# Optimization experiments

Hardware: AMD Instinct MI355X
Metric: run time of the kernel (lower is better)

Reference implementation:

```python
import jax, jax.numpy as jnp
import numpy as np

N, E, G, H, IN = 200000, 400000, 64, 128, 5
LN_EPS = 1e-5


def setup_inputs() -> dict:
    key = jax.random.key(0)
    ks = jax.random.split(key, 32)
    d = {}
    d["x"] = jax.random.normal(ks[0], (N, IN), jnp.float32)
    d["edge_index"] = jax.random.randint(ks[1], (2, E), 0, N, dtype=jnp.int32)
    d["edge_attr"] = jax.random.normal(ks[2], (E, 1), jnp.float32)
    d["batch"] = jnp.sort(jax.random.randint(ks[3], (N,), 0, G, dtype=jnp.int32))
    dims = [IN, H, H]
    i = 4
    names = [("ew", "eb", "w1_", "b1_", "w2_", "b2_", "g", "bt")]
    for l, din in enumerate(dims):
        d[f"ew{l}"] = jax.random.normal(ks[i], (1, din), jnp.float32); i += 1
        d[f"eb{l}"] = jnp.zeros((din,), jnp.float32)
        d[f"w1_{l}"] = jax.random.normal(ks[i], (din, H), jnp.float32) / np.sqrt(din); i += 1
        d[f"b1_{l}"] = jnp.zeros((H,), jnp.float32)
        d[f"w2_{l}"] = jax.random.normal(ks[i], (H, H), jnp.float32) / np.sqrt(H); i += 1
        d[f"b2_{l}"] = jnp.zeros((H,), jnp.float32)
        d[f"g{l}"] = jnp.ones((H,), jnp.float32)
        d[f"bt{l}"] = jnp.zeros((H,), jnp.float32)
    return d


def _gine_layer(x, src, dst, edge_attr, ew, eb, w1, b1, w2, b2, g, bt):
    # edge encoder: Linear(1, din)
    e = edge_attr @ ew + eb                       # [E, din]
    # GINEConv message: ReLU(x_j + e), aggregated (sum) at destination
    m = jax.nn.relu(x[src] + e)                   # [E, din]
    aggr = jax.ops.segment_sum(m, dst, num_segments=N)  # [N, din]
    h = x + aggr                                  # (1 + eps)*x with eps=0
    # GIN MLP: Linear -> ReLU -> Linear
    h = jax.nn.relu(h @ w1 + b1) @ w2 + b2        # [N, H]
    # LayerNorm
    mu = jnp.mean(h, axis=-1, keepdims=True)
    var = jnp.mean((h - mu) ** 2, axis=-1, keepdims=True)
    h = (h - mu) * jax.lax.rsqrt(var + LN_EPS) * g + bt
    return jax.nn.relu(h)


def reference(x, edge_index, edge_attr, batch,
              ew0, eb0, w1_0, b1_0, w2_0, b2_0, g0, bt0,
              ew1, eb1, w1_1, b1_1, w2_1, b2_1, g1, bt1,
              ew2, eb2, w1_2, b1_2, w2_2, b2_2, g2, bt2):
    src, dst = edge_index[0], edge_index[1]
    x = _gine_layer(x, src, dst, edge_attr, ew0, eb0, w1_0, b1_0, w2_0, b2_0, g0, bt0)
    x = _gine_layer(x, src, dst, edge_attr, ew1, eb1, w1_1, b1_1, w2_1, b2_1, g1, bt1)
    x = _gine_layer(x, src, dst, edge_attr, ew2, eb2, w1_2, b1_2, w2_2, b2_2, g2, bt2)
    # global pooling per graph
    add_pool = jax.ops.segment_sum(x, batch, num_segments=G)           # [G, H]
    counts = jax.ops.segment_sum(jnp.ones((N,), x.dtype), batch, num_segments=G)
    mean_pool = add_pool / jnp.maximum(counts, 1.0)[:, None]           # [G, H]
    return jnp.concatenate([mean_pool, add_pool], axis=1)              # [G, 2H]
```

## Files before the change

### kernel.cpp

```cpp
#include <hip/hip_runtime.h>

#define N_NODES 200000
#define N_EDGES 400000
#define N_GRAPHS 64
#define HDIM 128
#define INDIM 5
#define LN_EPS 1e-5f
#define LDA 138
#define NPBLK 64

typedef __attribute__((ext_vector_type(8))) short short8;
typedef __attribute__((ext_vector_type(4))) float f32x4;

__device__ __forceinline__ unsigned short to_bf(float v) {
    unsigned u = __builtin_bit_cast(unsigned, v);
    return (unsigned short)((u + 0x7FFFu + ((u >> 16) & 1u)) >> 16);
}
__device__ __forceinline__ float bf_lo(unsigned w) { return __builtin_bit_cast(float, w << 16); }
__device__ __forceinline__ float bf_hi(unsigned w) { return __builtin_bit_cast(float, w & 0xFFFF0000u); }
__device__ __forceinline__ float bf2f(unsigned short h) { return __builtin_bit_cast(float, (unsigned)h << 16); }


__global__ void hist_kernel(const int* __restrict__ ei, int* __restrict__ deg) {
    int e = blockIdx.x * blockDim.x + threadIdx.x;
    if (e < N_EDGES) atomicAdd(&deg[ei[N_EDGES + e]], 1);
}

#define SCAN_CHUNK 1024
#define SCAN_BLOCKS ((N_NODES + SCAN_CHUNK - 1) / SCAN_CHUNK)

__global__ __launch_bounds__(256) void scan_phaseA(const int* __restrict__ deg, int* __restrict__ bsums,
                                                   int* __restrict__ poolz) {
    if (blockIdx.x == 0) {
        for (int i = threadIdx.x; i < N_GRAPHS * HDIM + N_GRAPHS; i += 256) poolz[i] = 0;
    }
    __shared__ int red[256];
    int t = threadIdx.x;
    int base = blockIdx.x * SCAN_CHUNK + t * 4;
    int s = 0;
#pragma unroll
    for (int k = 0; k < 4; ++k) {
        int i = base + k;
        s += (i < N_NODES) ? deg[i] : 0;
    }
    red[t] = s;
    __syncthreads();
    for (int off = 128; off; off >>= 1) {
        if (t < off) red[t] += red[t + off];
        __syncthreads();
    }
    if (t == 0) bsums[blockIdx.x] = red[0];
}

__global__ __launch_bounds__(256) void scan_phaseB(int* __restrict__ bsums, int* __restrict__ row_ptr) {
    __shared__ int s[256];
    int t = threadIdx.x;
    int v = (t < SCAN_BLOCKS) ? bsums[t] : 0;
    s[t] = v;
    __syncthreads();
    for (int off = 1; off < 256; off <<= 1) {
        int add = (t >= off) ? s[t - off] : 0;
        __syncthreads();
        s[t] += add;
        __syncthreads();
    }
    if (t < SCAN_BLOCKS) bsums[t] = s[t] - v;
    if (t == SCAN_BLOCKS - 1) row_ptr[N_NODES] = s[t];
}

__global__ __launch_bounds__(256) void scan_phaseC(const int* __restrict__ deg,
                                                   const int* __restrict__ bsums,
                                                   int* __restrict__ row_ptr,
                                                   int* __restrict__ cursor) {
    __shared__ int ts[256];
    int t = threadIdx.x;
    int base = blockIdx.x * SCAN_CHUNK + t * 4;
    int v[4];
    int s = 0;
#pragma unroll
    for (int k = 0; k < 4; ++k) {
        int i = base + k;
        v[k] = (i < N_NODES) ? deg[i] : 0;
        s += v[k];
    }
    ts[t] = s;
    __syncthreads();
    for (int off = 1; off < 256; off <<= 1) {
        int add = (t >= off) ? ts[t - off] : 0;
        __syncthreads();
        ts[t] += add;
        __syncthreads();
    }
    int run = bsums[blockIdx.x] + ts[t] - s;
#pragma unroll
    for (int k = 0; k < 4; ++k) {
        int i = base + k;
        if (i < N_NODES) { row_ptr[i] = run; cursor[i] = 0; }
        run += v[k];
    }
}

#define SCATTER_BLOCKS ((N_EDGES + 255) / 256)

__global__ void scatter_pack(const int* __restrict__ ei, const float* __restrict__ ea,
                             const int* __restrict__ row_ptr, int* __restrict__ cursor,
                             int2* __restrict__ csr,
                             const float* __restrict__ s0, short* __restrict__ d0,
                             const float* __restrict__ s1, short* __restrict__ d1,
                             const float* __restrict__ s2, short* __restrict__ d2,
                             const float* __restrict__ s3, short* __restrict__ d3,
                             const float* __restrict__ s4, short* __restrict__ d4,
                             const float* __restrict__ s5, short* __restrict__ d5) {
    int b = blockIdx.x;
    if (b < SCATTER_BLOCKS) {
        int e = b * 256 + threadIdx.x;
        if (e >= N_EDGES) return;
        int d = ei[N_EDGES + e];
        int pos = atomicAdd(&cursor[d], 1);
        csr[row_ptr[d] + pos] = make_int2(ei[e], __float_as_int(ea[e]));
        return;
    }
    b -= SCATTER_BLOCKS;
    const float* W;
    short* D;
    int din, KP, b0;
    if (b < 16)       { W = s0; D = d0; din = 5;   KP = 32;  b0 = 0; }
    else if (b < 80)  { W = s1; D = d1; din = 128; KP = 128; b0 = 16; }
    else if (b < 144) { W = s2; D = d2; din = 128; KP = 128; b0 = 80; }
    else if (b < 208) { W = s3; D = d3; din = 128; KP = 128; b0 = 144; }
    else if (b < 272) { W = s4; D = d4; din = 128; KP = 128; b0 = 208; }
    else              { W = s5; D = d5; din = 128; KP = 128; b0 = 272; }
    int idx = (b - b0) * 256 + threadIdx.x;
    if (idx >= KP * 128) return;
    int j = idx & 7;
    int lane = (idx >> 3) & 63;
    int rest = idx >> 9;
    int KS = KP >> 5;
    int kstep = rest % KS;
    int tile = rest / KS;
    int k = kstep * 32 + ((lane >> 4) * 8) + j;
    int n = tile * 16 + (lane & 15);
    float v = (k < din) ? W[k * 128 + n] : 0.f;
    D[idx] = (short)to_bf(v);
}

template <int KP1, bool POOL>
__global__ __launch_bounds__(256, 4) void layer_fused(
    const void* __restrict__ xin_v, const int* __restrict__ row_ptr,
    const int2* __restrict__ csr,
    const float* __restrict__ ew, const float* __restrict__ eb,
    const short* __restrict__ w1h, const float* __restrict__ b1,
    const short* __restrict__ w2h, const float* __restrict__ b2,
    const float* __restrict__ g, const float* __restrict__ bt,
    unsigned short* __restrict__ xout,
    const int* __restrict__ batch, float* __restrict__ pool, int* __restrict__ cnt) {
    __shared__ __align__(16) unsigned short A16[NPBLK * LDA];
    __shared__ int bidx[NPBLK];
    union Scratch {
        float eweb[256];
        float part[NPBLK][4][INDIM];
    };
    __shared__ Scratch u;

    int tid = threadIdx.x;
    int node0 = blockIdx.x * NPBLK;

    if (KP1 == 128) {
        const unsigned short* xin = (const unsigned short*)xin_v;
        if (tid < 32) ((float4*)u.eweb)[tid] = ((const float4*)ew)[tid];
        else if (tid < 64) ((float4*)u.eweb)[tid] = ((const float4*)eb)[tid - 32];
        if (POOL && tid >= 64 && tid < 128) bidx[tid - 64] = batch[node0 + tid - 64];

        int row = tid >> 2, qt = tid & 3, c0 = qt * 32;
        int node = node0 + row;
        float acc[32];
        {
            const uint4* xn = (const uint4*)(xin + (size_t)node * 128 + c0);
            uint4 uv[4];
#pragma unroll
            for (int j = 0; j < 4; ++j) uv[j] = xn[j];
            unsigned wds[16] = {uv[0].x, uv[0].y, uv[0].z, uv[0].w,
                                uv[1].x, uv[1].y, uv[1].z, uv[1].w,
                                uv[2].x, uv[2].y, uv[2].z, uv[2].w,
                                uv[3].x, uv[3].y, uv[3].z, uv[3].w};
#pragma unroll
            for (int i = 0; i < 16; ++i) {
                acc[2 * i] = bf_lo(wds[i]);
                acc[2 * i + 1] = bf_hi(wds[i]);
            }
        }
        int beg = row_ptr[node], end = row_ptr[node + 1];
        __syncthreads();

        int2 r;
        if (beg < end) r = csr[beg];
        for (int e = beg; e < end; ++e) {
            int2 rn = (e + 1 < end) ? csr[e + 1] : r;
            float a = __int_as_float(r.y);
            const uint4* xs = (const uint4*)(xin + (size_t)r.x * 128 + c0);
            uint4 uv[4];
#pragma unroll
            for (int j = 0; j < 4; ++j) uv[j] = xs[j];
            unsigned wds[16] = {uv[0].x, uv[0].y, uv[0].z, uv[0].w,
                                uv[1].x, uv[1].y, uv[1].z, uv[1].w,
                                uv[2].x, uv[2].y, uv[2].z, uv[2].w,
                                uv[3].x, uv[3].y, uv[3].z, uv[3].w};
#pragma unroll
            for (int i = 0; i < 16; ++i) {
                int cA = c0 + 2 * i, cB = cA + 1;
                acc[2 * i] += fmaxf(fmaf(a, u.eweb[cA], bf_lo(wds[i]) + u.eweb[128 + cA]), 0.f);
                acc[2 * i + 1] += fmaxf(fmaf(a, u.eweb[cB], bf_hi(wds[i]) + u.eweb[128 + cB]), 0.f);
            }
            r = rn;
        }
        unsigned* Ar = (unsigned*)&A16[row * LDA + c0];
#pragma unroll
        for (int i = 0; i < 16; ++i)
            Ar[i] = (unsigned)to_bf(acc[2 * i]) | ((unsigned)to_bf(acc[2 * i + 1]) << 16);
    } else {
        const float* xinf = (const float*)xin_v;
        int row = tid >> 2, qt = tid & 3;
        int node = node0 + row;
        {
            float w[INDIM], b[INDIM], acc[INDIM];
#pragma unroll
            for (int j = 0; j < INDIM; ++j) {
                w[j] = ew[j];
                b[j] = eb[j];
                acc[j] = 0.f;
            }
            int beg = row_ptr[node], end = row_ptr[node + 1];
            int2 r;
            if (beg + qt < end) r = csr[beg + qt];
            for (int e = beg + qt; e < end; e += 4) {
                int2 rn = (e + 4 < end) ? csr[e + 4] : r;
                float a = __int_as_float(r.y);
#pragma unroll
                for (int j = 0; j < INDIM; ++j)
                    acc[j] += fmaxf(fmaf(a, w[j], xinf[r.x * INDIM + j] + b[j]), 0.f);
                r = rn;
            }
#pragma unroll
            for (int j = 0; j < INDIM; ++j) u.part[row][qt][j] = acc[j];
        }
        __syncthreads();
        if (tid < NPBLK) {
#pragma unroll
            for (int j = 0; j < INDIM; ++j) {
                float v = xinf[(node0 + tid) * INDIM + j] + u.part[tid][0][j] + u.part[tid][1][j] +
                          u.part[tid][2][j] + u.part[tid][3][j];
                A16[tid * LDA + j] = to_bf(v);
            }
#pragma unroll
            for (int j = INDIM; j < 32; ++j) A16[tid * LDA + j] = 0;
        }
        __syncthreads();
    }

    int wv = tid >> 6, lane = tid & 63;
    int mrow = lane & 15, q = lane >> 4;
    int arow = wv * 16 + mrow;

    const short8* w1p = (const short8*)w1h;
    const short8* w2p = (const short8*)w2h;

    f32x4 acc2[8];
#pragma unroll
    for (int t = 0; t < 8; ++t) acc2[t] = (f32x4){0.f, 0.f, 0.f, 0.f};
    constexpr int KS1 = KP1 / 32;
#pragma unroll
    for (int ks = 0; ks < KS1; ++ks) {
        short8 bh[8];
#pragma unroll
        for (int t = 0; t < 8; ++t) bh[t] = w1p[((size_t)t * KS1 + ks) * 64 + lane];
        short8 ah = *(const short8*)&A16[arow * LDA + ks * 32 + q * 8];
#pragma unroll
        for (int t = 0; t < 8; ++t)
            acc2[t] = __builtin_amdgcn_mfma_f32_16x16x32_bf16(ah, bh[t], acc2[t], 0, 0, 0);
    }
    {
        float b1v[8];
#pragma unroll
        for (int t = 0; t < 8; ++t) b1v[t] = b1[t * 16 + mrow];
#pragma unroll
        for (int t = 0; t < 8; ++t)
#pragma unroll
            for (int r = 0; r < 4; ++r) {
                int rrow = wv * 16 + q * 4 + r;
                int col = t * 16 + mrow;
                A16[rrow * LDA + col] = to_bf(fmaxf(acc2[t][r] + b1v[t], 0.f));
            }
    }

#pragma unroll
    for (int t = 0; t < 8; ++t) acc2[t] = (f32x4){0.f, 0.f, 0.f, 0.f};
#pragma unroll
    for (int ks = 0; ks < 4; ++ks) {
        short8 bh[8];
#pragma unroll
        for (int t = 0; t < 8; ++t) bh[t] = w2p[((size_t)t * 4 + ks) * 64 + lane];
        short8 ah = *(const short8*)&A16[arow * LDA + ks * 32 + q * 8];
#pragma unroll
        for (int t = 0; t < 8; ++t)
            acc2[t] = __builtin_amdgcn_mfma_f32_16x16x32_bf16(ah, bh[t], acc2[t], 0, 0, 0);
    }

    float s4[4] = {0.f, 0.f, 0.f, 0.f}, q4[4] = {0.f, 0.f, 0.f, 0.f};
    {
        float b2v[8];
#pragma unroll
        for (int t = 0; t < 8; ++t) b2v[t] = b2[t * 16 + mrow];
#pragma unroll
        for (int t = 0; t < 8; ++t)
#pragma unroll
            for (int r = 0; r < 4; ++r) {
                float v = acc2[t][r] + b2v[t];
                acc2[t][r] = v;
                s4[r] += v;
                q4[r] += v * v;
            }
    }
#pragma unroll
    for (int m = 1; m <= 8; m <<= 1) {
#pragma unroll
        for (int r = 0; r < 4; ++r) {
            s4[r] += __shfl_xor(s4[r], m, 64);
            q4[r] += __shfl_xor(q4[r], m, 64);
        }
    }
    float mu[4], inv[4];
#pragma unroll
    for (int r = 0; r < 4; ++r) {
        mu[r] = s4[r] * (1.f / HDIM);
        float var = q4[r] * (1.f / HDIM) - mu[r] * mu[r];
        inv[r] = rsqrtf(var + LN_EPS);
    }
    float gv[8], btv[8];
#pragma unroll
    for (int t = 0; t < 8; ++t) {
        gv[t] = g[t * 16 + mrow];
        btv[t] = bt[t * 16 + mrow];
    }

#pragma unroll
    for (int t = 0; t < 8; ++t)
#pragma unroll
        for (int r = 0; r < 4; ++r) {
            int rrow = wv * 16 + q * 4 + r;
            int col = t * 16 + mrow;
            float o = fmaxf((acc2[t][r] - mu[r]) * inv[r] * gv[t] + btv[t], 0.f);
            A16[rrow * LDA + col] = to_bf(o);
        }
    __syncthreads();

    if (!POOL) {
        unsigned* xo = (unsigned*)xout;
#pragma unroll
        for (int i = 0; i < 16; ++i) {
            int idx = tid + 256 * i;
            int row = idx >> 6, w = idx & 63;
            xo[(size_t)(node0 + row) * 64 + w] = ((const unsigned*)&A16[row * LDA])[w];
        }
    } else {
        if (tid < 128) {
            int col = tid;
            float accp = 0.f;
            int cur = bidx[0];
            for (int r = 0; r < NPBLK; ++r) {
                int gi = bidx[r];
                if (gi != cur) {
                    unsafeAtomicAdd(&pool[cur * HDIM + col], accp);
                    accp = 0.f;
                    cur = gi;
                }
                accp += bf2f(A16[r * LDA + col]);
            }
            unsafeAtomicAdd(&pool[cur * HDIM + col], accp);
        } else if (tid == 255) {
            int cur = bidx[0], c = 0;
            for (int r = 0; r < NPBLK; ++r) {
                if (bidx[r] != cur) {
                    atomicAdd(&cnt[cur], c);
                    c = 0;
                    cur = bidx[r];
                }
                ++c;
            }
            atomicAdd(&cnt[cur], c);
        }
    }
}

__global__ void pool_final(const float* __restrict__ pool, const int* __restrict__ cnt,
                           float* __restrict__ out) {
    int g = blockIdx.x, j = threadIdx.x;
    float add = pool[g * HDIM + j];
    float c = (float)max(cnt[g], 1);
    out[g * (2 * HDIM) + j] = add / c;
    out[g * (2 * HDIM) + HDIM + j] = add;
}

extern "C" void kernel_launch(void* const* d_in, const int* in_sizes, int n_in,
                              void* d_out, int out_size, void* d_ws, size_t ws_size,
                              hipStream_t stream) {
    const float* x_in = (const float*)d_in[0];
    const int* ei = (const int*)d_in[1];
    const float* ea = (const float*)d_in[2];
    const int* batch = (const int*)d_in[3];
    const float* P[24];
    for (int i = 0; i < 24; ++i) P[i] = (const float*)d_in[4 + i];

    unsigned short* x_a = (unsigned short*)d_ws;
    unsigned short* x_b = x_a + (size_t)N_NODES * HDIM;
    float* pool = (float*)(x_b + (size_t)N_NODES * HDIM);
    int* cnt = (int*)(pool + N_GRAPHS * HDIM);
    int* deg = cnt + N_GRAPHS;
    int* cursor = deg + N_NODES;
    int* row_ptr = cursor + N_NODES;
    int* bsums = row_ptr + N_NODES + 1;
    int2* csr = (int2*)(bsums + 256);
    short* wp = (short*)(((uintptr_t)(csr + N_EDGES) + 15) & ~(uintptr_t)15);
    float* out = (float*)d_out;

    short *w1h[3], *w2h[3];
    for (int l = 0; l < 3; ++l) {
        w1h[l] = wp + (size_t)l * 32768;
        w2h[l] = w1h[l] + 16384;
    }

    hipMemsetAsync(deg, 0, N_NODES * sizeof(int), stream);

    hist_kernel<<<(N_EDGES + 255) / 256, 256, 0, stream>>>(ei, deg);
    scan_phaseA<<<SCAN_BLOCKS, 256, 0, stream>>>(deg, bsums, (int*)pool);
    scan_phaseB<<<1, 256, 0, stream>>>(bsums, row_ptr);
    scan_phaseC<<<SCAN_BLOCKS, 256, 0, stream>>>(deg, bsums, row_ptr, cursor);

    scatter_pack<<<SCATTER_BLOCKS + 336, 256, 0, stream>>>(
        ei, ea, row_ptr, cursor, csr,
        P[2], w1h[0], P[4], w2h[0],
        P[10], w1h[1], P[12], w2h[1],
        P[18], w1h[2], P[20], w2h[2]);

    layer_fused<32, false><<<N_NODES / NPBLK, 256, 0, stream>>>(
        x_in, row_ptr, csr, P[0], P[1],
        w1h[0], P[3], w2h[0], P[5], P[6], P[7], x_a, nullptr, nullptr, nullptr);
    layer_fused<128, false><<<N_NODES / NPBLK, 256, 0, stream>>>(
        x_a, row_ptr, csr, P[8], P[9],
        w1h[1], P[11], w2h[1], P[13], P[14], P[15], x_b, nullptr, nullptr, nullptr);
    layer_fused<128, true><<<N_NODES / NPBLK, 256, 0, stream>>>(
        x_b, row_ptr, csr, P[16], P[17],
        w1h[2], P[19], w2h[2], P[21], P[22], P[23], nullptr, batch, pool, cnt);

    pool_final<<<N_GRAPHS, HDIM, 0, stream>>>(pool, cnt, out);
}
```

Before: 344.3 us.

## Double-buffer neighbor gathers, pack edge params, use packed bf16 convert

```diff
diff --git a/kernel.cpp b/kernel.cpp
--- a/kernel.cpp
+++ b/kernel.cpp
@@ -6,11 +6,12 @@
 #define HDIM 128
 #define INDIM 5
 #define LN_EPS 1e-5f
-#define LDA 138
+#define LDA 140
 #define NPBLK 64
 
 typedef __attribute__((ext_vector_type(8))) short short8;
 typedef __attribute__((ext_vector_type(4))) float f32x4;
+typedef __attribute__((ext_vector_type(2))) float f32x2;
 
 __device__ __forceinline__ unsigned short to_bf(float v) {
     unsigned u = __builtin_bit_cast(unsigned, v);
@@ -19,6 +20,48 @@
 __device__ __forceinline__ float bf_lo(unsigned w) { return __builtin_bit_cast(float, w << 16); }
 __device__ __forceinline__ float bf_hi(unsigned w) { return __builtin_bit_cast(float, w & 0xFFFF0000u); }
 __device__ __forceinline__ float bf2f(unsigned short h) { return __builtin_bit_cast(float, (unsigned)h << 16); }
+
+__device__ __forceinline__ unsigned short cvt1_bf(float v) {
+    unsigned r;
+    asm("v_cvt_pk_bf16_f32 %0, %1, %1" : "=v"(r) : "v"(v));
+    return (unsigned short)r;
+}
+__device__ __forceinline__ unsigned cvt2_bf(float lo, float hi) {
+    unsigned r;
+    asm("v_cvt_pk_bf16_f32 %0, %1, %2" : "=v"(r) : "v"(lo), "v"(hi));
+    return r;
+}
+__device__ __forceinline__ f32x2 vmax0(f32x2 v) {
+#if __has_builtin(__builtin_elementwise_max)
+    return __builtin_elementwise_max(v, (f32x2)0.f);
+#else
+    v.x = fmaxf(v.x, 0.f);
+    v.y = fmaxf(v.y, 0.f);
+    return v;
+#endif
+}
+
+__device__ __forceinline__ void gproc(uint4 w0, uint4 w1, uint4 w2, uint4 w3, float a_,
+                                      const float4* ep, f32x2* accv) {
+    unsigned ws[16] = {w0.x, w0.y, w0.z, w0.w, w1.x, w1.y, w1.z, w1.w,
+                       w2.x, w2.y, w2.z, w2.w, w3.x, w3.y, w3.z, w3.w};
+    f32x2 av = a_;
+#pragma unroll
+    for (int p = 0; p < 16; ++p) {
+        float4 wb = ep[p];
+        f32x2 xv;
+        xv.x = bf_lo(ws[p]);
+        xv.y = bf_hi(ws[p]);
+        f32x2 ew2, eb2;
+        ew2.x = wb.x;
+        ew2.y = wb.y;
+        eb2.x = wb.z;
+        eb2.y = wb.w;
+        f32x2 t = xv + eb2;
+        t = av * ew2 + t;
+        accv[p] += vmax0(t);
+    }
+}
 
 
 __global__ void hist_kernel(const int* __restrict__ ei, int* __restrict__ deg) {
@@ -157,66 +200,83 @@
     __shared__ __align__(16) unsigned short A16[NPBLK * LDA];
     __shared__ int bidx[NPBLK];
     union Scratch {
-        float eweb[256];
-        float part[NPBLK][4][INDIM];
+        float eweb4[4 * 17 * 4];
+        float part[KP1 == 128 ? 1 : NPBLK][4][INDIM];
     };
-    __shared__ Scratch u;
+    __shared__ __align__(16) Scratch u;
 
     int tid = threadIdx.x;
     int node0 = blockIdx.x * NPBLK;
 
-    if (KP1 == 128) {
+    if constexpr (KP1 == 128) {
         const unsigned short* xin = (const unsigned short*)xin_v;
-        if (tid < 32) ((float4*)u.eweb)[tid] = ((const float4*)ew)[tid];
-        else if (tid < 64) ((float4*)u.eweb)[tid] = ((const float4*)eb)[tid - 32];
+        if (tid < 64) {
+            int qq = tid >> 4, ii = tid & 15, c = qq * 32 + ii * 2;
+            ((float4*)u.eweb4)[qq * 17 + ii] = make_float4(ew[c], ew[c + 1], eb[c], eb[c + 1]);
+        }
         if (POOL && tid >= 64 && tid < 128) bidx[tid - 64] = batch[node0 + tid - 64];
 
         int row = tid >> 2, qt = tid & 3, c0 = qt * 32;
         int node = node0 + row;
-        float acc[32];
+
+        const uint4* xn = (const uint4*)(xin + (size_t)node * 128 + c0);
+        uint4 own0 = xn[0], own1 = xn[1], own2 = xn[2], own3 = xn[3];
+        int beg = row_ptr[node], end = row_ptr[node + 1];
+
+        int2 rA, rB;
+        uint4 a0, a1, a2, a3, b0, b1v4, b2v4, b3;
+        if (beg < end) {
+            rA = csr[beg];
+            const uint4* xs = (const uint4*)(xin + (size_t)rA.x * 128 + c0);
+            a0 = xs[0]; a1 = xs[1]; a2 = xs[2]; a3 = xs[3];
+        }
+        if (beg + 1 < end) {
+            rB = csr[beg + 1];
+            const uint4* xs = (const uint4*)(xin + (size_t)rB.x * 128 + c0);
+            b0 = xs[0]; b1v4 = xs[1]; b2v4 = xs[2]; b3 = xs[3];
+        }
+        __syncthreads();
+        const float4* ep = ((const float4*)u.eweb4) + qt * 17;
+
+        f32x2 accv[16];
         {
-            const uint4* xn = (const uint4*)(xin + (size_t)node * 128 + c0);
-            uint4 uv[4];
-#pragma unroll
-            for (int j = 0; j < 4; ++j) uv[j] = xn[j];
-            unsigned wds[16] = {uv[0].x, uv[0].y, uv[0].z, uv[0].w,
-                                uv[1].x, uv[1].y, uv[1].z, uv[1].w,
-                                uv[2].x, uv[2].y, uv[2].z, uv[2].w,
-                                uv[3].x, uv[3].y, uv[3].z, uv[3].w};
-#pragma unroll
-            for (int i = 0; i < 16; ++i) {
-                acc[2 * i] = bf_lo(wds[i]);
-                acc[2 * i + 1] = bf_hi(wds[i]);
-            }
-        }
-        int beg = row_ptr[node], end = row_ptr[node + 1];
-        __syncthreads();
-
-        int2 r;
-        if (beg < end) r = csr[beg];
-        for (int e = beg; e < end; ++e) {
-            int2 rn = (e + 1 < end) ? csr[e + 1] : r;
-            float a = __int_as_float(r.y);
-            const uint4* xs = (const uint4*)(xin + (size_t)r.x * 128 + c0);
-            uint4 uv[4];
-#pragma unroll
-            for (int j = 0; j < 4; ++j) uv[j] = xs[j];
-            unsigned wds[16] = {uv[0].x, uv[0].y, uv[0].z, uv[0].w,
-                                uv[1].x, uv[1].y, uv[1].z, uv[1].w,
-                                uv[2].x, uv[2].y, uv[2].z, uv[2].w,
-                                uv[3].x, uv[3].y, uv[3].z, uv[3].w};
-#pragma unroll
-            for (int i = 0; i < 16; ++i) {
-                int cA = c0 + 2 * i, cB = cA + 1;
-                acc[2 * i] += fmaxf(fmaf(a, u.eweb[cA], bf_lo(wds[i]) + u.eweb[128 + cA]), 0.f);
-                acc[2 * i + 1] += fmaxf(fmaf(a, u.eweb[cB], bf_hi(wds[i]) + u.eweb[128 + cB]), 0.f);
-            }
-            r = rn;
-        }
-        unsigned* Ar = (unsigned*)&A16[row * LDA + c0];
-#pragma unroll
-        for (int i = 0; i < 16; ++i)
-            Ar[i] = (unsigned)to_bf(acc[2 * i]) | ((unsigned)to_bf(acc[2 * i + 1]) << 16);
+            unsigned ws[16] = {own0.x, own0.y, own0.z, own0.w, own1.x, own1.y, own1.z, own1.w,
+                               own2.x, own2.y, own2.z, own2.w, own3.x, own3.y, own3.z, own3.w};
+#pragma unroll
+            for (int p = 0; p < 16; ++p) {
+                accv[p].x = bf_lo(ws[p]);
+                accv[p].y = bf_hi(ws[p]);
+            }
+        }
+
+        int e = beg;
+        while (e + 1 < end) {
+            int2 rN = rA, rM = rB;
+            bool hasN = (e + 2 < end), hasM = (e + 3 < end);
+            if (hasN) rN = csr[e + 2];
+            if (hasM) rM = csr[e + 3];
+            gproc(a0, a1, a2, a3, __int_as_float(rA.y), ep, accv);
+            if (hasN) {
+                const uint4* xs = (const uint4*)(xin + (size_t)rN.x * 128 + c0);
+                a0 = xs[0]; a1 = xs[1]; a2 = xs[2]; a3 = xs[3];
+            }
+            gproc(b0, b1v4, b2v4, b3, __int_as_float(rB.y), ep, accv);
+            if (hasM) {
+                const uint4* xs = (const uint4*)(xin + (size_t)rM.x * 128 + c0);
+                b0 = xs[0]; b1v4 = xs[1]; b2v4 = xs[2]; b3 = xs[3];
+            }
+            rA = rN;
+            rB = rM;
+            e += 2;
+        }
+        if (e < end) gproc(a0, a1, a2, a3, __int_as_float(rA.y), ep, accv);
+
+        uint2* Ar2 = (uint2*)&A16[row * LDA + c0];
+#pragma unroll
+        for (int k = 0; k < 8; ++k) {
+            Ar2[k] = make_uint2(cvt2_bf(accv[2 * k].x, accv[2 * k].y),
+                                cvt2_bf(accv[2 * k + 1].x, accv[2 * k + 1].y));
+        }
     } else {
         const float* xinf = (const float*)xin_v;
         int row = tid >> 2, qt = tid & 3;
@@ -249,7 +309,7 @@
             for (int j = 0; j < INDIM; ++j) {
                 float v = xinf[(node0 + tid) * INDIM + j] + u.part[tid][0][j] + u.part[tid][1][j] +
                           u.part[tid][2][j] + u.part[tid][3][j];
-                A16[tid * LDA + j] = to_bf(v);
+                A16[tid * LDA + j] = cvt1_bf(v);
             }
 #pragma unroll
             for (int j = INDIM; j < 32; ++j) A16[tid * LDA + j] = 0;
@@ -288,7 +348,7 @@
             for (int r = 0; r < 4; ++r) {
                 int rrow = wv * 16 + q * 4 + r;
                 int col = t * 16 + mrow;
-                A16[rrow * LDA + col] = to_bf(fmaxf(acc2[t][r] + b1v[t], 0.f));
+                A16[rrow * LDA + col] = cvt1_bf(fmaxf(acc2[t][r] + b1v[t], 0.f));
             }
     }
 
@@ -349,7 +409,7 @@
             int rrow = wv * 16 + q * 4 + r;
             int col = t * 16 + mrow;
             float o = fmaxf((acc2[t][r] - mu[r]) * inv[r] * gv[t] + btv[t], 0.f);
-            A16[rrow * LDA + col] = to_bf(o);
+            A16[rrow * LDA + col] = cvt1_bf(o);
         }
     __syncthreads();
 
```

After: 877.6 us. +154.9%, slower.
